# Optimization experiments

Measured on AMD Instinct MI355X. Metric: run time of the kernel, lower is better.

## Reference

```python
import jax, jax.numpy as jnp
import numpy as np

# Dims: module math forces per-head depth D == num_points == N (see analysis).
B, H, N = 4, 8, 1024
D = N                      # q_depth = k_depth = v_depth = num_points
C_IN = 64                  # q_in = k_in = v_in
C_OUT = H * D              # q_out = k_out = v_out = 8192
SCALE = float(np.sqrt(D))


def _split_heads(t):
    # t: [B, C_OUT, N] -> view(B, H, D, N) -> permute -> [B, H, N, D]
    return t.reshape(B, H, D, N).transpose(0, 1, 3, 2)


def setup_inputs() -> dict:
    key = jax.random.key(0)
    ks = jax.random.split(key, 9)
    s = 0.02
    return {
        "coordinate": jax.random.normal(ks[0], (B, 3, N), jnp.float32),
        "x": jax.random.normal(ks[1], (B, C_IN, N, 1), jnp.float32),
        "neighbors": jax.random.normal(ks[2], (B, C_IN, N, 1), jnp.float32),
        # 1x1 Conv2d weights (out, in), no bias
        "Wq": jax.random.normal(ks[3], (C_OUT, C_IN), jnp.float32) * s,
        "Wk": jax.random.normal(ks[4], (C_OUT, C_IN), jnp.float32) * s,
        "Wv": jax.random.normal(ks[5], (C_OUT, C_IN), jnp.float32) * s,
        # nn.Linear(3, q_out) / nn.Linear(3, v_out)
        "Wlq": jax.random.normal(ks[6], (C_OUT, 3), jnp.float32) * s,
        "blq": jnp.zeros((C_OUT,), jnp.float32),
        "Wlv": jax.random.normal(ks[7], (C_OUT, 3), jnp.float32) * s,
        "blv": jnp.zeros((C_OUT,), jnp.float32),
    }


def reference(coordinate, x, neighbors, Wq, Wk, Wv, Wlq, blq, Wlv, blv):
    # Att_Score_method='dot_product', pos_method='method_ii' (hardcoded branch)
    xs = x[..., 0]           # [B, C_IN, N]  (squeeze trailing Conv2d width dim)
    ns = neighbors[..., 0]   # [B, C_IN, N]

    q = _split_heads(jnp.einsum('oc,bcn->bon', Wq, xs))  # [B,H,N,D]
    k = _split_heads(jnp.einsum('oc,bcn->bon', Wk, ns))  # [B,H,N,D]
    v = _split_heads(jnp.einsum('oc,bcn->bon', Wv, ns))  # [B,H,N,D]

    coords = coordinate.transpose(0, 2, 1)               # [B, N, 3]
    # positional encodings, split into heads: [B,H,N,D]
    pos_q = _split_heads((coords @ Wlq.T + blq).transpose(0, 2, 1))
    pos_v = _split_heads((coords @ Wlv.T + blv).transpose(0, 2, 1))

    # q_context = q @ pos_q^T ; energy = q @ k^T + q_context  -> [B,H,N,N]
    q_context = jnp.einsum('bhnd,bhmd->bhnm', q, pos_q)
    energy = jnp.einsum('bhnd,bhmd->bhnm', q, k) + q_context

    attn = jax.nn.softmax(energy / SCALE, axis=-1)       # [B,H,N,N]
    v_context = v + pos_v                                 # [B,H,N,D], D==N
    out = attn * v_context                                # elementwise combine

    # permute(0,2,1,3) -> [B,N,H,D] -> reshape [B,N,H*D] -> permute -> [B,H*D,N]
    out = out.transpose(0, 2, 1, 3).reshape(B, N, H * D).transpose(0, 2, 1)
    return out
```

## Files before the change

### kernel.cpp

```cpp
#include <hip/hip_runtime.h>

#define NN 1024
#define KP 96
#define LSTR 104

typedef __attribute__((ext_vector_type(8))) short short8;
typedef __attribute__((ext_vector_type(4))) short short4v;
typedef __attribute__((ext_vector_type(4))) float f32x4;

__device__ __forceinline__ short f2bf(float f){
  unsigned u = __builtin_bit_cast(unsigned, f);
  u += 0x7FFFu + ((u >> 16) & 1u);
  return (short)(u >> 16);
}

__global__ __launch_bounds__(256) void prep_all(
    const float* __restrict__ Wq, const float* __restrict__ Wk,
    const float* __restrict__ Wlq, const float* __restrict__ blq,
    const float* __restrict__ ns, const float* __restrict__ coord,
    const float* __restrict__ Wv, const float* __restrict__ Wlv,
    const float* __restrict__ blv,
    short* __restrict__ PTbf, short* __restrict__ Bm, short* __restrict__ Vm){
  __shared__ union SU {
    float red[4][64][9];
    struct { float nsT[64][65]; float cst[3][64]; } bb;
  } S;
  const int t = threadIdx.x;
  const int r = blockIdx.x;

  if (r < 96){
    const int h = r / 12, kidx = r % 12, kk0 = kidx * 8;
    const int c = t & 63, p = t >> 6;
    if (kidx > 8){
      if (p == 0){
        #pragma unroll
        for (int j = 0; j < 8; ++j) PTbf[(h*96 + kk0 + j)*64 + c] = 0;
      }
      return;
    }
    float acc[8];
    #pragma unroll
    for (int j = 0; j < 8; ++j) acc[j] = 0.f;
    if (kidx < 8){
      #pragma unroll 4
      for (int i = 0; i < 256; ++i){
        const int o = h*1024 + p*256 + i;
        const float wq = Wq[o*64 + c];
        const float* wk = Wk + o*64 + kk0;
        f32x4 b0 = *(const f32x4*)(wk);
        f32x4 b1 = *(const f32x4*)(wk + 4);
        #pragma unroll
        for (int j = 0; j < 4; ++j){ acc[j] += wq*b0[j]; acc[4+j] += wq*b1[j]; }
      }
    } else {
      #pragma unroll 4
      for (int i = 0; i < 256; ++i){
        const int o = h*1024 + p*256 + i;
        const float wq = Wq[o*64 + c];
        acc[0] += wq * Wlq[o*3 + 0];
        acc[1] += wq * Wlq[o*3 + 1];
        acc[2] += wq * Wlq[o*3 + 2];
        acc[3] += wq * blq[o];
      }
    }
    #pragma unroll
    for (int j = 0; j < 8; ++j) S.red[p][c][j] = acc[j];
    __syncthreads();
    if (p == 0){
      #pragma unroll
      for (int j = 0; j < 8; ++j){
        float s = S.red[0][c][j] + S.red[1][c][j] + S.red[2][c][j] + S.red[3][c][j];
        PTbf[(h*96 + kk0 + j)*64 + c] = f2bf(s);
      }
    }
  } else if (r < 160){
    const int rb = r - 96;
    const int b = rb >> 4, m0 = (rb & 15) * 64;
    #pragma unroll
    for (int it = 0; it < 16; ++it){
      int idx = it * 256 + t;
      int c = idx >> 6, mm = idx & 63;
      S.bb.nsT[mm][c] = ns[(b*64 + c)*NN + m0 + mm];
    }
    if (t < 192){
      int j = t >> 6, mm = t & 63;
      S.bb.cst[j][mm] = coord[(b*3 + j)*NN + m0 + mm];
    }
    __syncthreads();
    #pragma unroll
    for (int it = 0; it < 24; ++it){
      int idx = it * 256 + t;
      int mm = idx / KP, kk = idx - mm*KP;
      float v = (kk < 64) ? S.bb.nsT[mm][kk]
              : (kk < 67) ? S.bb.cst[kk - 64][mm]
              : (kk == 67) ? 1.f : 0.f;
      Bm[(b*NN + m0 + mm)*KP + kk] = f2bf(v);
    }
  } else {
    const int o0 = (r - 160) * 64;
    #pragma unroll
    for (int it = 0; it < 24; ++it){
      int idx = it * 256 + t;
      int rr = idx / KP, kk = idx - rr*KP;
      int o = o0 + rr;
      float v = (kk < 64) ? Wv[o*64 + kk]
              : (kk < 67) ? Wlv[o*3 + (kk - 64)]
              : (kk == 67) ? blv[o] : 0.f;
      Vm[o*KP + kk] = f2bf(v);
    }
  }
}

__global__ __launch_bounds__(512, 4) void attn_main(
    const float* __restrict__ xs, const short* __restrict__ PTbf,
    const short* __restrict__ Bmat, const short* __restrict__ Vm,
    float* __restrict__ out){
  __shared__ short xsL[64 * 64];
  __shared__ short AL[64 * LSTR];
  __shared__ short BL[64 * LSTR];
  __shared__ float redS[64 * 9];
  __shared__ float rinvS[64];
  const int t = threadIdx.x, w = t >> 6, lane = t & 63;
  const int q = lane >> 4, ln = lane & 15;
  const int blk0 = blockIdx.x;
  const int blk = (blk0 & 7) * 64 + (blk0 >> 3);
  const int nb = blk & 15, bh = blk >> 4;
  const int b = bh >> 3, h = bh & 7;
  const int n0 = nb * 64;

  const float* xsb = xs + b * 64 * NN;
  #pragma unroll
  for (int it = 0; it < 2; ++it){
    int idx = it * 512 + t;
    int c = idx >> 4, nn4 = (idx & 15) << 2;
    f32x4 v = *(const f32x4*)(xsb + c * NN + n0 + nn4);
    short4v pk;
    #pragma unroll
    for (int j = 0; j < 4; ++j) pk[j] = f2bf(v[j]);
    *(short4v*)(&xsL[c * 64 + nn4]) = pk;
  }
  const short* Bb = Bmat + b * NN * KP;
  #pragma unroll
  for (int it = 0; it < 2; ++it){
    int idx = it * 512 + t;
    if (idx < 768){
      int row = idx / 12, s8 = idx - row * 12;
      *(short8*)(&BL[row * LSTR + s8 * 8]) =
          *(const short8*)(Bb + (n0 + row) * KP + s8 * 8);
    }
  }
  __syncthreads();

  {
    const int rw = (w & 3) * 16, kh = w >> 2;
    short8 xf0, xf1;
    #pragma unroll
    for (int j = 0; j < 8; ++j){
      xf0[j] = xsL[(q * 8 + j) * 64 + rw + ln];
      xf1[j] = xsL[(32 + q * 8 + j) * 64 + rw + ln];
    }
    const short* PTh = PTbf + h * KP * 64;
    #pragma unroll
    for (int j = 0; j < 3; ++j){
      int kt = kh * 3 + j;
      const short* pr = PTh + (kt * 16 + ln) * 64;
      short8 p0 = *(const short8*)(pr + q * 8);
      short8 p1 = *(const short8*)(pr + 32 + q * 8);
      f32x4 a = {0.f, 0.f, 0.f, 0.f};
      a = __builtin_amdgcn_mfma_f32_16x16x32_bf16(xf0, p0, a, 0, 0, 0);
      a = __builtin_amdgcn_mfma_f32_16x16x32_bf16(xf1, p1, a, 0, 0, 0);
      #pragma unroll
      for (int r = 0; r < 4; ++r)
        AL[(rw + q * 4 + r) * LSTR + kt * 16 + ln] = f2bf(a[r]);
    }
  }
  __syncthreads();

  short8 af[4][3];
  #pragma unroll
  for (int rf = 0; rf < 4; ++rf)
    #pragma unroll
    for (int s = 0; s < 3; ++s)
      af[rf][s] = *(const short8*)(&AL[(rf * 16 + ln) * LSTR + s * 32 + q * 8]);
  const float KEXP = 0.045084220f;

  float sum[4][4];
  #pragma unroll
  for (int rf = 0; rf < 4; ++rf)
    #pragma unroll
    for (int r = 0; r < 4; ++r) sum[rf][r] = 0.f;

  {
    const short* bp = Bb + (w * 128 + ln) * KP + q * 8;
    for (int ms = 0; ms < 8; ++ms){
      short8 bf0 = *(const short8*)(bp);
      short8 bf1 = *(const short8*)(bp + 32);
      short8 bf2 = *(const short8*)(bp + 64);
      bp += 16 * KP;
      #pragma unroll
      for (int rf = 0; rf < 4; ++rf){
        f32x4 e = {0.f, 0.f, 0.f, 0.f};
        e = __builtin_amdgcn_mfma_f32_16x16x32_bf16(af[rf][0], bf0, e, 0, 0, 0);
        e = __builtin_amdgcn_mfma_f32_16x16x32_bf16(af[rf][1], bf1, e, 0, 0, 0);
        e = __builtin_amdgcn_mfma_f32_16x16x32_bf16(af[rf][2], bf2, e, 0, 0, 0);
        #pragma unroll
        for (int r = 0; r < 4; ++r)
          sum[rf][r] += __builtin_amdgcn_exp2f(e[r] * KEXP);
      }
    }
  }
  #pragma unroll
  for (int rf = 0; rf < 4; ++rf){
    #pragma unroll
    for (int r = 0; r < 4; ++r){
      float s = sum[rf][r];
      s += __shfl_xor(s, 1); s += __shfl_xor(s, 2);
      s += __shfl_xor(s, 4); s += __shfl_xor(s, 8);
      if (ln == 0) redS[(rf * 16 + q * 4 + r) * 9 + w] = s;
    }
  }
  __syncthreads();
  if (t < 64){
    float s = 0.f;
    #pragma unroll
    for (int ww = 0; ww < 8; ++ww) s += redS[t * 9 + ww];
    rinvS[t] = 1.0f / s;
  }
  __syncthreads();

  {
    const short* Vh = Vm + h * 1024 * KP;
    const short* bp = Bb + (w * 128 + ln) * KP + q * 8;
    const short* vp = Vh + (w * 128 + ln) * KP + q * 8;
    float* op = out + (size_t)bh * (1024 * 1024) + (w * 128 + ln) * NN + n0;
    for (int ds = 0; ds < 8; ++ds){
      short8 bf0 = *(const short8*)(bp);
      short8 bf1 = *(const short8*)(bp + 32);
      short8 bf2 = *(const short8*)(bp + 64);
      short8 vf0 = *(const short8*)(vp);
      short8 vf1 = *(const short8*)(vp + 32);
      short8 vf2 = *(const short8*)(vp + 64);
      bp += 16 * KP; vp += 16 * KP;
      #pragma unroll
      for (int rf = 0; rf < 4; ++rf){
        const short* blp = &BL[(rf * 16 + ln) * LSTR + q * 8];
        short8 bn0 = *(const short8*)(blp);
        short8 bn1 = *(const short8*)(blp + 32);
        short8 bn2 = *(const short8*)(blp + 64);
        f32x4 e  = {0.f, 0.f, 0.f, 0.f};
        f32x4 vv = {0.f, 0.f, 0.f, 0.f};
        e  = __builtin_amdgcn_mfma_f32_16x16x32_bf16(af[rf][0], bf0, e, 0, 0, 0);
        e  = __builtin_amdgcn_mfma_f32_16x16x32_bf16(af[rf][1], bf1, e, 0, 0, 0);
        e  = __builtin_amdgcn_mfma_f32_16x16x32_bf16(af[rf][2], bf2, e, 0, 0, 0);
        vv = __builtin_amdgcn_mfma_f32_16x16x32_bf16(bn0, vf0, vv, 0, 0, 0);
        vv = __builtin_amdgcn_mfma_f32_16x16x32_bf16(bn1, vf1, vv, 0, 0, 0);
        vv = __builtin_amdgcn_mfma_f32_16x16x32_bf16(bn2, vf2, vv, 0, 0, 0);
        f32x4 ri = *(const f32x4*)(&rinvS[rf * 16 + q * 4]);
        f32x4 o;
        #pragma unroll
        for (int r = 0; r < 4; ++r)
          o[r] = __builtin_amdgcn_exp2f(e[r] * KEXP) * ri[r] * vv[r];
        *(f32x4*)(op + rf * 16 + q * 4) = o;
      }
      op += 16 * NN;
    }
  }
}

extern "C" void kernel_launch(void* const* d_in, const int* in_sizes, int n_in,
                              void* d_out, int out_size, void* d_ws, size_t ws_size,
                              hipStream_t stream){
  const float* coord = (const float*)d_in[0];
  const float* x     = (const float*)d_in[1];
  const float* nbr   = (const float*)d_in[2];
  const float* Wq    = (const float*)d_in[3];
  const float* Wk    = (const float*)d_in[4];
  const float* Wv    = (const float*)d_in[5];
  const float* Wlq   = (const float*)d_in[6];
  const float* blq   = (const float*)d_in[7];
  const float* Wlv   = (const float*)d_in[8];
  const float* blv   = (const float*)d_in[9];
  float* out = (float*)d_out;

  char* ws = (char*)d_ws;
  short* PTbf = (short*)ws;
  short* Bm   = (short*)(ws + 98304);
  short* Vm   = (short*)(ws + 98304 + 786432);

  prep_all<<<288, 256, 0, stream>>>(Wq, Wk, Wlq, blq, nbr, coord, Wv, Wlv, blv,
                                    PTbf, Bm, Vm);
  attn_main<<<512, 512, 0, stream>>>(x, PTbf, Bm, Vm, out);
}
```

Measured before the change: 245.9 us.

## Stage output tiles through swizzled LDS for coalesced stores and swizzle BL layout

Each wave now writes its 16x64 fp32 output tile into a per-wave shared buffer with an XOR swizzle, then reads it back so each store instruction covers four full 256-byte rows instead of many scattered 64-byte segments. The B tile in LDS changes from a padded stride to a 128-element row with an XOR-swizzled chunk index, to cut bank conflicts on the fragment reads. The per-row reciprocal sums are loaded into registers once, outside the loop. The output staging buffer shares memory with the now-dead xs/A tiles through a union, but total LDS per block still grows, which may lower the number of resident blocks.

```diff
diff --git a/kernel.cpp b/kernel.cpp
--- a/kernel.cpp
+++ b/kernel.cpp
@@ -115,9 +115,11 @@
     const float* __restrict__ xs, const short* __restrict__ PTbf,
     const short* __restrict__ Bmat, const short* __restrict__ Vm,
     float* __restrict__ out){
-  __shared__ short xsL[64 * 64];
-  __shared__ short AL[64 * LSTR];
-  __shared__ short BL[64 * LSTR];
+  __shared__ union UT {
+    struct { short xsL[64 * 64]; short AL[64 * LSTR]; } s;
+    float OT[8][16 * 64];
+  } U;
+  __shared__ short BL[64 * 128];
   __shared__ float redS[64 * 9];
   __shared__ float rinvS[64];
   const int t = threadIdx.x, w = t >> 6, lane = t & 63;
@@ -137,7 +139,7 @@
     short4v pk;
     #pragma unroll
     for (int j = 0; j < 4; ++j) pk[j] = f2bf(v[j]);
-    *(short4v*)(&xsL[c * 64 + nn4]) = pk;
+    *(short4v*)(&U.s.xsL[c * 64 + nn4]) = pk;
   }
   const short* Bb = Bmat + b * NN * KP;
   #pragma unroll
@@ -145,7 +147,8 @@
     int idx = it * 512 + t;
     if (idx < 768){
       int row = idx / 12, s8 = idx - row * 12;
-      *(short8*)(&BL[row * LSTR + s8 * 8]) =
+      int phys = s8 ^ (row & 7);
+      *(short8*)(&BL[row * 128 + phys * 8]) =
           *(const short8*)(Bb + (n0 + row) * KP + s8 * 8);
     }
   }
@@ -156,8 +159,8 @@
     short8 xf0, xf1;
     #pragma unroll
     for (int j = 0; j < 8; ++j){
-      xf0[j] = xsL[(q * 8 + j) * 64 + rw + ln];
-      xf1[j] = xsL[(32 + q * 8 + j) * 64 + rw + ln];
+      xf0[j] = U.s.xsL[(q * 8 + j) * 64 + rw + ln];
+      xf1[j] = U.s.xsL[(32 + q * 8 + j) * 64 + rw + ln];
     }
     const short* PTh = PTbf + h * KP * 64;
     #pragma unroll
@@ -171,7 +174,7 @@
       a = __builtin_amdgcn_mfma_f32_16x16x32_bf16(xf1, p1, a, 0, 0, 0);
       #pragma unroll
       for (int r = 0; r < 4; ++r)
-        AL[(rw + q * 4 + r) * LSTR + kt * 16 + ln] = f2bf(a[r]);
+        U.s.AL[(rw + q * 4 + r) * LSTR + kt * 16 + ln] = f2bf(a[r]);
     }
   }
   __syncthreads();
@@ -181,7 +184,7 @@
   for (int rf = 0; rf < 4; ++rf)
     #pragma unroll
     for (int s = 0; s < 3; ++s)
-      af[rf][s] = *(const short8*)(&AL[(rf * 16 + ln) * LSTR + s * 32 + q * 8]);
+      af[rf][s] = *(const short8*)(&U.s.AL[(rf * 16 + ln) * LSTR + s * 32 + q * 8]);
   const float KEXP = 0.045084220f;
 
   float sum[4][4];
@@ -228,11 +231,18 @@
   }
   __syncthreads();
 
+  f32x4 rinv[4];
+  #pragma unroll
+  for (int rf = 0; rf < 4; ++rf)
+    rinv[rf] = *(const f32x4*)(&rinvS[rf * 16 + q * 4]);
+
   {
     const short* Vh = Vm + h * 1024 * KP;
     const short* bp = Bb + (w * 128 + ln) * KP + q * 8;
     const short* vp = Vh + (w * 128 + ln) * KP + q * 8;
-    float* op = out + (size_t)bh * (1024 * 1024) + (w * 128 + ln) * NN + n0;
+    float* ot = U.OT[w];
+    float* obase = out + (size_t)bh * (1024 * 1024) + n0;
+    const int k7 = ln & 7;
     for (int ds = 0; ds < 8; ++ds){
       short8 bf0 = *(const short8*)(bp);
       short8 bf1 = *(const short8*)(bp + 32);
@@ -243,10 +253,10 @@
       bp += 16 * KP; vp += 16 * KP;
       #pragma unroll
       for (int rf = 0; rf < 4; ++rf){
-        const short* blp = &BL[(rf * 16 + ln) * LSTR + q * 8];
-        short8 bn0 = *(const short8*)(blp);
-        short8 bn1 = *(const short8*)(blp + 32);
-        short8 bn2 = *(const short8*)(blp + 64);
+        const short* blp = &BL[(rf * 16 + ln) * 128];
+        short8 bn0 = *(const short8*)(blp + (((q    ) ^ k7) << 3));
+        short8 bn1 = *(const short8*)(blp + (((4 | q) ^ k7) << 3));
+        short8 bn2 = *(const short8*)(blp + (((8 | q) ^ k7) << 3));
         f32x4 e  = {0.f, 0.f, 0.f, 0.f};
         f32x4 vv = {0.f, 0.f, 0.f, 0.f};
         e  = __builtin_amdgcn_mfma_f32_16x16x32_bf16(af[rf][0], bf0, e, 0, 0, 0);
@@ -255,14 +265,18 @@
         vv = __builtin_amdgcn_mfma_f32_16x16x32_bf16(bn0, vf0, vv, 0, 0, 0);
         vv = __builtin_amdgcn_mfma_f32_16x16x32_bf16(bn1, vf1, vv, 0, 0, 0);
         vv = __builtin_amdgcn_mfma_f32_16x16x32_bf16(bn2, vf2, vv, 0, 0, 0);
-        f32x4 ri = *(const f32x4*)(&rinvS[rf * 16 + q * 4]);
         f32x4 o;
         #pragma unroll
         for (int r = 0; r < 4; ++r)
-          o[r] = __builtin_amdgcn_exp2f(e[r] * KEXP) * ri[r] * vv[r];
-        *(f32x4*)(op + rf * 16 + q * 4) = o;
-      }
-      op += 16 * NN;
+          o[r] = __builtin_amdgcn_exp2f(e[r] * KEXP) * rinv[rf][r] * vv[r];
+        *(f32x4*)(&ot[(ln << 6) + (((rf * 4 + q) ^ ln) << 2)]) = o;
+      }
+      #pragma unroll
+      for (int j = 0; j < 4; ++j){
+        int rr = j * 4 + q;
+        f32x4 v = *(const f32x4*)(&ot[(rr << 6) + ((ln ^ rr) << 2)]);
+        *(f32x4*)(obase + (size_t)(w * 128 + ds * 16 + rr) * NN + (ln << 2)) = v;
+      }
     }
   }
 }
```

Result: slower. 299.1 us (+21.6%).
